# Kernel tuning notes

Hardware: AMD Instinct MI355X
Metric: run time of the kernel (lower is better)

Reference implementation:

```python
import jax, jax.numpy as jnp
import numpy as np
import math

EPS = 1e-12


def _cmul(ar, ai, br, bi):
    return ar * br - ai * bi, ar * bi + ai * br


def _wilson_seed(x):
    # x: (B, 4, L, L) -> conj of canonical Wilson-line path, (B, L, L) re/im
    ux_r, ux_i, uy_r, uy_i = x[:, 0], x[:, 1], x[:, 2], x[:, 3]
    B, L, _ = ux_r.shape
    dt = x.dtype

    def step(c, u):
        cr, ci = c
        ur, ui = u
        nr, ni = _cmul(cr, ci, ur, ui)
        return (nr, ni), (nr, ni)

    # cumulative complex product along x at y=0
    init_r = jnp.ones((B,), dt)
    init_i = jnp.zeros((B,), dt)
    xs = (ux_r[:, :-1, 0].T, ux_i[:, :-1, 0].T)  # (L-1, B)
    _, (axr, axi) = jax.lax.scan(step, (init_r, init_i), xs)
    x_axis_r = jnp.concatenate([init_r[None], axr], 0).T  # (B, L)
    x_axis_i = jnp.concatenate([init_i[None], axi], 0).T

    # cumulative complex product along y, vectorized over x
    ys = (jnp.moveaxis(uy_r[:, :, :-1], 2, 0), jnp.moveaxis(uy_i[:, :, :-1], 2, 0))  # (L-1, B, L)
    _, (pr, pi_) = jax.lax.scan(step, (x_axis_r, x_axis_i), ys)
    path_r = jnp.moveaxis(jnp.concatenate([x_axis_r[None], pr], 0), 0, 2)  # (B, L, L)
    path_i = jnp.moveaxis(jnp.concatenate([x_axis_i[None], pi_], 0), 0, 2)
    return path_r, -path_i  # conjugate


def _wrap(t):
    return (t + math.pi) % (2.0 * math.pi) - math.pi


def _initial_features(x):
    seed_r, seed_i = _wilson_seed(x)
    ax = jnp.arctan2(x[:, 1], x[:, 0])
    ay = jnp.arctan2(x[:, 3], x[:, 2])
    plaq = _wrap(ax + jnp.roll(ay, -1, axis=1) - jnp.roll(ax, -1, axis=2) - ay)
    pc = jnp.cos(plaq)
    pavg = (pc + jnp.roll(pc, 1, 1) + jnp.roll(pc, -1, 1)
            + jnp.roll(pc, 1, 2) + jnp.roll(pc, -1, 2)) / 5.0
    scalars = jnp.stack([jnp.ones_like(pc), pc, pavg], axis=1)  # (B, 3, L, L)
    return seed_r[:, None] * scalars, seed_i[:, None] * scalars


def _transport_fwd(fr, fi, x, mu):
    lr, li = (x[:, 0], x[:, 1]) if mu == 0 else (x[:, 2], x[:, 3])
    sr = jnp.roll(fr, -1, axis=mu + 2)
    si = jnp.roll(fi, -1, axis=mu + 2)
    return _cmul(lr[:, None], li[:, None], sr, si)


def _transport_bwd(fr, fi, x, mu):
    lr, li = (x[:, 0], x[:, 1]) if mu == 0 else (x[:, 2], x[:, 3])
    cr = jnp.roll(lr, 1, axis=mu + 1)
    ci = jnp.roll(-li, 1, axis=mu + 1)
    sr = jnp.roll(fr, 1, axis=mu + 2)
    si = jnp.roll(fi, 1, axis=mu + 2)
    return _cmul(cr[:, None], ci[:, None], sr, si)


def _lconv(fr, fi, x, center, fwd_w, bwd_w):
    out_r = jnp.einsum('oi,bixy->boxy', center, fr)
    out_i = jnp.einsum('oi,bixy->boxy', center, fi)
    for mu in range(2):
        fr2, fi2 = _transport_fwd(fr, fi, x, mu)
        br2, bi2 = _transport_bwd(fr, fi, x, mu)
        out_r = out_r + jnp.einsum('oi,bixy->boxy', fwd_w[mu], fr2) \
                      + jnp.einsum('oi,bixy->boxy', bwd_w[mu], br2)
        out_i = out_i + jnp.einsum('oi,bixy->boxy', fwd_w[mu], fi2) \
                      + jnp.einsum('oi,bixy->boxy', bwd_w[mu], bi2)
    return out_r, out_i


def _modrelu(fr, fi, bias):
    mag = jnp.sqrt(fr * fr + fi * fi + EPS)
    act = jax.nn.relu(mag + bias[None, :, None, None])
    scale = act / jnp.maximum(mag, EPS)
    return fr * scale, fi * scale


def setup_inputs() -> dict:
    key = jax.random.key(0)
    ks = jax.random.split(key, 11)
    B, L, H, O = 64, 128, 16, 8
    s = 0.1
    return {
        'x': jax.random.normal(ks[0], (B, 4, L, L), jnp.float32),
        'center1': s * jax.random.normal(ks[1], (H, 3), jnp.float32),
        'fwd_w1': s * jax.random.normal(ks[2], (2, H, 3), jnp.float32),
        'bwd_w1': s * jax.random.normal(ks[3], (2, H, 3), jnp.float32),
        'bias1': jnp.zeros((H,), jnp.float32),
        'center2': s * jax.random.normal(ks[4], (O, H), jnp.float32),
        'fwd_w2': s * jax.random.normal(ks[5], (2, O, H), jnp.float32),
        'bwd_w2': s * jax.random.normal(ks[6], (2, O, H), jnp.float32),
        'bias2': jnp.zeros((O,), jnp.float32),
        'ro_weight': s * jax.random.normal(ks[7], (O,), jnp.float32),
        'ro_bias': jnp.zeros((1,), jnp.float32),
    }


def reference(x, center1, fwd_w1, bwd_w1, bias1, center2, fwd_w2, bwd_w2, bias2, ro_weight, ro_bias):
    fr, fi = _initial_features(x)
    fr, fi = _lconv(fr, fi, x, center1, fwd_w1, bwd_w1)
    fr, fi = _modrelu(fr, fi, bias1)
    fr, fi = _lconv(fr, fi, x, center2, fwd_w2, bwd_w2)
    fr, fi = _modrelu(fr, fi, bias2)
    inv = fr * fr + fi * fi
    return jnp.einsum('c,bcxy->bxy', ro_weight, inv)[:, None] + ro_bias.reshape(1, 1, 1, 1)
```

## Files before the change

### kernel.cpp

```cpp
#include <hip/hip_runtime.h>
#include <math.h>

#define LQ   128
#define BQ   64
#define LL   (LQ*LQ)
#define H1   16
#define O2   8
#define TILE 16
#define REG  18
#define NPTS (REG*REG)
#define PCR  22
#define PCN  (PCR*PCR)
#define LKR  23
#define LKN  (LKR*LKR)

typedef float f2 __attribute__((ext_vector_type(2)));
using bf8 = __attribute__((ext_vector_type(8))) short;
using f4  = __attribute__((ext_vector_type(4))) float;

__device__ __forceinline__ int wrapi(int v) { return v & (LQ - 1); }

__device__ __forceinline__ unsigned pack_bf(float hi, float lo) {
    return __builtin_amdgcn_perm(__float_as_uint(hi), __float_as_uint(lo),
                                 0x07060302u);
}
__device__ __forceinline__ unsigned cvt_pk_bf16(float lo, float hi) {
    unsigned r;
    asm("v_cvt_pk_bf16_f32 %0, %1, %2" : "=v"(r) : "v"(lo), "v"(hi));
    return r;
}

#define WS_W1 ((size_t)BQ * LL)

__global__ __launch_bounds__(256)
void k_scan(const float* __restrict__ x,
            const float* __restrict__ c1, const float* __restrict__ fw1,
            const float* __restrict__ bw1, float* __restrict__ ws) {
    int blk = blockIdx.x;
    if (blk == BQ * 8) {
        int tid = threadIdx.x;
        if (tid < 120) {
            int t = tid / 24, r = tid - t * 24;
            int c = r >> 3, op = r & 7;
            const float* src = (t == 0) ? c1 : (t == 1) ? fw1 : (t == 2) ? bw1
                             : (t == 3) ? (fw1 + 48) : (bw1 + 48);
            float2 v = make_float2(src[(2 * op) * 3 + c], src[(2 * op + 1) * 3 + c]);
            ((float2*)ws)[WS_W1 + tid] = v;
        }
        return;
    }
    int b = blk >> 3, rq = blk & 7;
    int l = threadIdx.x & 63, w = threadIdx.x >> 6;
    const float* x0 = x + (size_t)b * 4 * LL;
    const float* x1 = x0 + LL;

    float ur0 = x0[(2 * l) * LQ],     ui0 = x1[(2 * l) * LQ];
    float ur1 = x0[(2 * l + 1) * LQ], ui1 = x1[(2 * l + 1) * LQ];
    float pr = ur0 * ur1 - ui0 * ui1;
    float pi = ur0 * ui1 + ui0 * ur1;
    for (int d = 1; d < 64; d <<= 1) {
        float qr = __shfl_up(pr, d, 64);
        float qi = __shfl_up(pi, d, 64);
        if (l >= d) {
            float nr = qr * pr - qi * pi;
            float ni = qr * pi + qi * pr;
            pr = nr; pi = ni;
        }
    }
    float er = __shfl_up(pr, 1, 64);
    float ei = __shfl_up(pi, 1, 64);
    if (l == 0) { er = 1.f; ei = 0.f; }
    float e1r = er * ur0 - ei * ui0;
    float e1i = er * ui0 + ei * ur0;

    const float* yrp = x + (size_t)(b * 4 + 2) * LL;
    const float* yip = yrp + LL;
    float4* seed4 = (float4*)ws;

    for (int k = 0; k < 4; ++k) {
        int i = rq * 16 + w * 4 + k;
        float cxr = __shfl((i & 1) ? e1r : er, i >> 1, 64);
        float cxi = __shfl((i & 1) ? e1i : ei, i >> 1, 64);
        const float* yr = yrp + (size_t)i * LQ;
        const float* yi = yip + (size_t)i * LQ;
        float vr0 = yr[2 * l],     vi0 = yi[2 * l];
        float vr1 = yr[2 * l + 1], vi1 = yi[2 * l + 1];
        float sr = vr0 * vr1 - vi0 * vi1;
        float si = vr0 * vi1 + vi0 * vr1;
        for (int d = 1; d < 64; d <<= 1) {
            float qr = __shfl_up(sr, d, 64);
            float qi = __shfl_up(si, d, 64);
            if (l >= d) {
                float nr = qr * sr - qi * si;
                float ni = qr * si + qi * sr;
                sr = nr; si = ni;
            }
        }
        float gr = __shfl_up(sr, 1, 64);
        float gi = __shfl_up(si, 1, 64);
        if (l == 0) { gr = 1.f; gi = 0.f; }
        float s0r = cxr * gr - cxi * gi;
        float s0i = cxr * gi + cxi * gr;
        float s1r = s0r * vr0 - s0i * vi0;
        float s1i = s0r * vi0 + s0i * vr0;
        seed4[((size_t)b * LL + (size_t)i * LQ) / 2 + l] =
            make_float4(s0r, -s0i, s1r, -s1i);
    }
}

__global__ __launch_bounds__(256, 5)
void k_main(const float* __restrict__ x,
            const float* __restrict__ c2, const float* __restrict__ fw2,
            const float* __restrict__ bw2, const float* __restrict__ b1,
            const float* __restrict__ b2,
            const float* __restrict__ ro, const float* __restrict__ rob,
            const float* __restrict__ ws, float* __restrict__ out) {
    __shared__ __align__(16) unsigned s_f1[NPTS * 16];
    __shared__ f2 s_ux[LKN];
    __shared__ f2 s_uy[LKN];
    __shared__ float s_pc[PCN];
    int tid = threadIdx.x;
    int b = blockIdx.z, i0 = blockIdx.y * TILE, j0 = blockIdx.x * TILE;
    const float* x0 = x + (size_t)b * 4 * LL;
    const float* x1 = x0 + LL;
    const float* x2 = x0 + 2 * LL;
    const float* x3 = x0 + 3 * LL;
    const float2* seed = (const float2*)ws + (size_t)b * LL;
    const float2* W1 = (const float2*)ws + WS_W1;

    int lane = tid & 63, w = tid >> 6;
    int kc = lane >> 4, h = lane & 15, half = kc >> 1;

    bool z1 = true;
#pragma unroll
    for (int hh = 0; hh < H1; ++hh) z1 = z1 && (b1[hh] == 0.f);
    bool z2 = true;
#pragma unroll
    for (int oo = 0; oo < O2; ++oo) z2 = z2 && (b2[oo] == 0.f);

    bf8 a1 = {0, 0, 0, 0, 0, 0, 0, 0};
    if (kc < 2) {
        float v[8];
#pragma unroll
        for (int j = 0; j < 8; ++j) {
            int k = kc * 8 + j;
            float val = 0.f;
            if (k < 15) {
                int q = k / 3, c = k - q * 3;
                val = ((const float*)(W1 + (q * 24 + c * 8 + (h >> 1))))[h & 1];
            }
            v[j] = val;
        }
        unsigned dw[4];
#pragma unroll
        for (int d = 0; d < 4; ++d) dw[d] = cvt_pk_bf16(v[2 * d], v[2 * d + 1]);
        __builtin_memcpy(&a1, dw, 16);
    }

    for (int p = tid; p < LKN; p += 256) {
        int ri = p / LKR, rj = p - ri * LKR;
        int gi = wrapi(i0 - 3 + ri), gj = wrapi(j0 - 3 + rj);
        int idx = gi * LQ + gj;
        s_ux[p] = (f2){x0[idx], x1[idx]};
        s_uy[p] = (f2){x2[idx], x3[idx]};
    }
    __syncthreads();

    for (int p = tid; p < PCN; p += 256) {
        int ri = p / PCR, rj = p - ri * PCR;
        int lb = ri * LKR + rj;
        f2 u1 = s_ux[lb];
        f2 u2 = s_uy[lb + LKR];
        f2 u3 = s_ux[lb + 1];
        f2 u4 = s_uy[lb];
        float ar = u1.x * u2.x - u1.y * u2.y, ai = u1.x * u2.y + u1.y * u2.x;
        float br = ar * u3.x + ai * u3.y,     bi = -ar * u3.y + ai * u3.x;
        float zr = br * u4.x + bi * u4.y,     zi = -br * u4.y + bi * u4.x;
        s_pc[p] = zr * __frsqrt_rn(fmaf(zr, zr, zi * zi) + 1e-30f);
    }
    __syncthreads();

    for (int wp = w * 64; wp < NPTS; wp += 256) {
        int p = wp + lane;
        int pp = (p < NPTS) ? p : (NPTS - 1);
        int ri = pp / REG, rj = pp - ri * REG;
        int lb = (ri + 2) * LKR + (rj + 2);
        int cb = (ri + 2) * PCR + (rj + 2);

        int gi0 = wrapi(i0 - 1 + ri), gim = wrapi(i0 - 2 + ri), gip = wrapi(i0 + ri);
        int gj0 = wrapi(j0 - 1 + rj), gjm = wrapi(j0 - 2 + rj), gjp = wrapi(j0 + rj);
        float2 SC  = seed[gi0 * LQ + gj0];
        float2 SXP = seed[gip * LQ + gj0];
        float2 SXM = seed[gim * LQ + gj0];
        float2 SYP = seed[gi0 * LQ + gjp];
        float2 SYM = seed[gi0 * LQ + gjm];

        f2 lx = s_ux[lb], ly = s_uy[lb];
        f2 mx = s_ux[lb - LKR], my = s_uy[lb - 1];
        float tr[5], ti[5], tc[5], tv[5];
        tr[0] = SC.x;                          ti[0] = SC.y;
        tr[1] = lx.x * SXP.x - lx.y * SXP.y;   ti[1] = lx.x * SXP.y + lx.y * SXP.x;
        tr[2] = mx.x * SXM.x + mx.y * SXM.y;   ti[2] = mx.x * SXM.y - mx.y * SXM.x;
        tr[3] = ly.x * SYP.x - ly.y * SYP.y;   ti[3] = ly.x * SYP.y + ly.y * SYP.x;
        tr[4] = my.x * SYM.x + my.y * SYM.y;   ti[4] = my.x * SYM.y - my.y * SYM.x;

        float p00 = s_pc[cb];
        float pP0 = s_pc[cb + PCR],     pM0 = s_pc[cb - PCR];
        float p0P = s_pc[cb + 1],       p0M = s_pc[cb - 1];
        float pP20 = s_pc[cb + 2*PCR],  pM20 = s_pc[cb - 2*PCR];
        float p0P2 = s_pc[cb + 2],      p0M2 = s_pc[cb - 2];
        float pPP = s_pc[cb + PCR + 1], pPM = s_pc[cb + PCR - 1];
        float pMP = s_pc[cb - PCR + 1], pMM = s_pc[cb - PCR - 1];
        tc[0] = p00; tc[1] = pP0; tc[2] = pM0; tc[3] = p0P; tc[4] = p0M;
        tv[0] = (p00 + pP0 + pM0 + p0P + p0M) * 0.2f;
        tv[1] = (pP0 + pP20 + p00 + pPP + pPM) * 0.2f;
        tv[2] = (pM0 + p00 + pM20 + pMP + pMM) * 0.2f;
        tv[3] = (p0P + pPP + pMP + p0P2 + p00) * 0.2f;
        tv[4] = (p0M + pPM + pMM + p00 + p0M2) * 0.2f;

        unsigned fr8[8], fi8[8];
        {
            float Fr[16], Fi[16];
#pragma unroll
            for (int q = 0; q < 5; ++q) {
                Fr[3*q]   = tr[q];         Fi[3*q]   = ti[q];
                Fr[3*q+1] = tc[q]*tr[q];   Fi[3*q+1] = tc[q]*ti[q];
                Fr[3*q+2] = tv[q]*tr[q];   Fi[3*q+2] = tv[q]*ti[q];
            }
            Fr[15] = 0.f; Fi[15] = 0.f;
#pragma unroll
            for (int d = 0; d < 8; ++d) {
                fr8[d] = cvt_pk_bf16(Fr[2*d], Fr[2*d+1]);
                fi8[d] = cvt_pk_bf16(Fi[2*d], Fi[2*d+1]);
            }
        }

        int ng = (NPTS - wp + 15) >> 4;
        if (ng > 4) ng = 4;
        for (int g = 0; g < ng; ++g) {
            int src = g * 16 + h;
            unsigned brw[4], biw[4];
#pragma unroll
            for (int d = 0; d < 4; ++d) {
                unsigned rlo = __shfl(fr8[d],     src, 64);
                unsigned rhi = __shfl(fr8[d + 4], src, 64);
                unsigned ilo = __shfl(fi8[d],     src, 64);
                unsigned ihi = __shfl(fi8[d + 4], src, 64);
                brw[d] = (kc == 0) ? rlo : ((kc == 1) ? rhi : 0u);
                biw[d] = (kc == 0) ? ilo : ((kc == 1) ? ihi : 0u);
            }
            bf8 br, bi;
            __builtin_memcpy(&br, brw, 16);
            __builtin_memcpy(&bi, biw, 16);
            f4 zc = {0.f, 0.f, 0.f, 0.f};
            f4 Dr = __builtin_amdgcn_mfma_f32_16x16x32_bf16(a1, br, zc, 0, 0, 0);
            f4 Di = __builtin_amdgcn_mfma_f32_16x16x32_bf16(a1, bi, zc, 0, 0, 0);
            int P = wp + g * 16 + h;
            if (P < NPTS) {
                if (!z1) {
#pragma unroll
                    for (int r = 0; r < 4; ++r) {
                        float q2 = Dr[r]*Dr[r] + Di[r]*Di[r] + 1e-12f;
                        float s = fmaxf(fmaf(b1[4*kc + r], __frsqrt_rn(q2), 1.f), 0.f);
                        Dr[r] *= s; Di[r] *= s;
                    }
                }
                unsigned pr0 = cvt_pk_bf16(Dr[0], Dr[1]);
                unsigned pr1 = cvt_pk_bf16(Dr[2], Dr[3]);
                unsigned pi0 = cvt_pk_bf16(Di[0], Di[1]);
                unsigned pi1 = cvt_pk_bf16(Di[2], Di[3]);
                int rot = (P >> 1) & 3;
                int base = P * 16 + ((kc & 1) << 1);
                int ar = base + ((((kc >> 1) + rot) & 3) << 2);
                int ai = base + ((((kc >> 1) + 2 + rot) & 3) << 2);
                *(uint2*)&s_f1[ar] = make_uint2(pr0, pr1);
                *(uint2*)&s_f1[ai] = make_uint2(pi0, pi1);
            }
        }
    }
    __syncthreads();

    const float* wLo[3] = {c2, bw2, bw2 + O2 * H1};
    const float* wHi[3] = {fw2, fw2 + O2 * H1, (const float*)0};
    bf8 afr[3];
#pragma unroll
    for (int pq = 0; pq < 3; ++pq) {
        bf8 z = {0, 0, 0, 0, 0, 0, 0, 0};
        const float* wsrc = half ? wHi[pq] : wLo[pq];
        int wrow = half ? (h - 8) : h;
        bool valid = half ? (h >= 8 && wsrc != 0) : (h < 8);
        if (valid) {
            const float* wp2 = wsrc + wrow * H1 + (kc & 1) * 8;
            float4 wa = *(const float4*)wp2;
            float4 wb = *(const float4*)(wp2 + 4);
            uint4 u;
            u.x = pack_bf(wa.y, wa.x);
            u.y = pack_bf(wa.w, wa.z);
            u.z = pack_bf(wb.y, wb.x);
            u.w = pack_bf(wb.w, wb.z);
            __builtin_memcpy(&z, &u, 16);
        }
        afr[pq] = z;
    }
    float4 ro_lo = *(const float4*)ro;
    float4 ro_hi = *(const float4*)(ro + 4);
    float4 b2_lo = *(const float4*)b2;
    float4 b2_hi = *(const float4*)(b2 + 4);
    float4 zf4 = make_float4(0.f, 0.f, 0.f, 0.f);
    float4 rv = (kc == 0) ? ro_lo : ((kc == 1) ? ro_hi : zf4);
    float4 bv = (kc == 0) ? b2_lo : ((kc == 1) ? b2_hi : zf4);
    float rob0 = rob[0];

    for (int g = 0; g < 4; ++g) {
        int row = w * 4 + g;
        int posc = (row + 1) * REG + (h + 1);
        int lb2 = (row + 3) * LKR + (h + 3);
        f2 lx = s_ux[lb2], ly = s_uy[lb2];
        f2 mx = s_ux[lb2 - LKR], my = s_uy[lb2 - 1];

        float Lr[3], Li[3];
        Lr[0] = half ? lx.x : 1.f;   Li[0] = half ? lx.y : 0.f;
        Lr[1] = half ? ly.x : mx.x;  Li[1] = half ? ly.y : -mx.y;
        Lr[2] = half ? 0.f : my.x;   Li[2] = half ? 0.f : -my.y;
        int dpl[3];
        dpl[0] = half ? REG : 0;
        dpl[1] = half ? 1 : -REG;
        dpl[2] = -1;

        f4 a2r = {0.f, 0.f, 0.f, 0.f}, a2i = {0.f, 0.f, 0.f, 0.f};
#pragma unroll
        for (int pq = 0; pq < 3; ++pq) {
            int posc2 = posc + dpl[pq];
            int rot2 = (posc2 >> 1) & 3;
            int bb = posc2 * 16;
            uint4 ur = *(const uint4*)&s_f1[bb + ((((kc & 1) + rot2) & 3) << 2)];
            uint4 ui = *(const uint4*)&s_f1[bb + ((((kc & 1) + 2 + rot2) & 3) << 2)];
            bf8 br, bi;
            __builtin_memcpy(&br, &ur, 16);
            __builtin_memcpy(&bi, &ui, 16);
            f4 zc = {0.f, 0.f, 0.f, 0.f};
            f4 sr = __builtin_amdgcn_mfma_f32_16x16x32_bf16(afr[pq], br, zc, 0, 0, 0);
            f4 si = __builtin_amdgcn_mfma_f32_16x16x32_bf16(afr[pq], bi, zc, 0, 0, 0);
            a2r += Lr[pq] * sr - Li[pq] * si;
            a2i += Lr[pq] * si + Li[pq] * sr;
        }

#pragma unroll
        for (int c = 0; c < 4; ++c) {
            a2r[c] += __shfl_xor(a2r[c], 32, 64);
            a2i[c] += __shfl_xor(a2i[c], 32, 64);
        }

        f4 q4 = a2r * a2r + a2i * a2i;
        float res;
        if (z2) {
            res = rv.x * q4.x + rv.y * q4.y + rv.z * q4.z + rv.w * q4.w;
        } else {
            float bvv[4] = {bv.x, bv.y, bv.z, bv.w};
            float rvv[4] = {rv.x, rv.y, rv.z, rv.w};
            res = 0.f;
#pragma unroll
            for (int r = 0; r < 4; ++r) {
                float qq = q4[r];
                float s = fmaxf(fmaf(bvv[r], __frsqrt_rn(qq + 1e-12f), 1.f), 0.f);
                res = fmaf(rvv[r], s * s * qq, res);
            }
        }
        res += __shfl_xor(res, 16, 64);
        if (kc == 0)
            out[(size_t)b * LL + (size_t)(i0 + row) * LQ + (j0 + h)] = res + rob0;
    }
}

extern "C" void kernel_launch(void* const* d_in, const int* in_sizes, int n_in,
                              void* d_out, int out_size, void* d_ws, size_t ws_size,
                              hipStream_t stream) {
    const float* x   = (const float*)d_in[0];
    const float* c1  = (const float*)d_in[1];
    const float* fw1 = (const float*)d_in[2];
    const float* bw1 = (const float*)d_in[3];
    const float* b1  = (const float*)d_in[4];
    const float* c2  = (const float*)d_in[5];
    const float* fw2 = (const float*)d_in[6];
    const float* bw2 = (const float*)d_in[7];
    const float* b2  = (const float*)d_in[8];
    const float* ro  = (const float*)d_in[9];
    const float* rob = (const float*)d_in[10];
    float* out = (float*)d_out;
    float* ws  = (float*)d_ws;

    k_scan<<<BQ * 8 + 1, 256, 0, stream>>>(x, c1, fw1, bw1, ws);
    dim3 grid(LQ / TILE, LQ / TILE, BQ);
    k_main<<<grid, 256, 0, stream>>>(x, c2, fw2, bw2, b1, b2,
                                     ro, rob, ws, out);
}
```

Baseline: 133.5 us.

## Widen main kernel to 512 threads, prepack bf16 weights, split feature build from MFMA

Both layers' weights are now converted to bf16 MFMA fragments once in the scan kernel's spare block and loaded directly by each lane. The main kernel moves to 512 threads, and the first-layer stage is split into two parts. A per-point feature build writes hi/lo bf16-split features to a wider, rotated shared buffer. A separate wave-distributed MFMA pass then reads them, replacing the earlier shuffle-based gather. The hi/lo split roughly doubles shared-memory traffic and storage for the features, and adds an extra barrier. In exchange it aims for higher parallelism and less per-block weight setup.

```diff
diff --git a/kernel.cpp b/kernel.cpp
--- a/kernel.cpp
+++ b/kernel.cpp
@@ -7,8 +7,13 @@
 #define H1   16
 #define O2   8
 #define TILE 16
+#define NTHR 512
+#define NWAVE 8
+#define RPW  2
 #define REG  18
 #define NPTS (REG*REG)
+#define NPTS_PAD 336
+#define NGRP 21
 #define PCR  22
 #define PCN  (PCR*PCR)
 #define LKR  23
@@ -20,32 +25,63 @@
 
 __device__ __forceinline__ int wrapi(int v) { return v & (LQ - 1); }
 
-__device__ __forceinline__ unsigned pack_bf(float hi, float lo) {
-    return __builtin_amdgcn_perm(__float_as_uint(hi), __float_as_uint(lo),
-                                 0x07060302u);
-}
 __device__ __forceinline__ unsigned cvt_pk_bf16(float lo, float hi) {
     unsigned r;
     asm("v_cvt_pk_bf16_f32 %0, %1, %2" : "=v"(r) : "v"(lo), "v"(hi));
     return r;
 }
 
-#define WS_W1 ((size_t)BQ * LL)
+#define WS_WF ((size_t)2 * BQ * LL)
 
 __global__ __launch_bounds__(256)
 void k_scan(const float* __restrict__ x,
             const float* __restrict__ c1, const float* __restrict__ fw1,
-            const float* __restrict__ bw1, float* __restrict__ ws) {
+            const float* __restrict__ bw1,
+            const float* __restrict__ c2, const float* __restrict__ fw2,
+            const float* __restrict__ bw2, float* __restrict__ ws) {
     int blk = blockIdx.x;
     if (blk == BQ * 8) {
         int tid = threadIdx.x;
-        if (tid < 120) {
-            int t = tid / 24, r = tid - t * 24;
-            int c = r >> 3, op = r & 7;
-            const float* src = (t == 0) ? c1 : (t == 1) ? fw1 : (t == 2) ? bw1
-                             : (t == 3) ? (fw1 + 48) : (bw1 + 48);
-            float2 v = make_float2(src[(2 * op) * 3 + c], src[(2 * op + 1) * 3 + c]);
-            ((float2*)ws)[WS_W1 + tid] = v;
+        uint4* wf = (uint4*)(ws + WS_WF);
+        if (tid < 64) {
+            int kc = tid >> 4, h = tid & 15;
+            unsigned dw[4];
+            float v[8];
+#pragma unroll
+            for (int j = 0; j < 8; ++j) {
+                int k = (kc & 1) * 8 + j;
+                float val = 0.f;
+                if (k < 15) {
+                    int q = k / 3, c = k - q * 3;
+                    const float* src = (q == 0) ? c1 : (q == 1) ? fw1
+                                     : (q == 2) ? bw1 : (q == 3) ? (fw1 + 48)
+                                     : (bw1 + 48);
+                    val = src[h * 3 + c];
+                }
+                v[j] = val;
+            }
+#pragma unroll
+            for (int d = 0; d < 4; ++d) dw[d] = cvt_pk_bf16(v[2*d], v[2*d+1]);
+            uint4 u = {dw[0], dw[1], dw[2], dw[3]};
+            wf[tid] = u;
+        } else {
+            int idx = tid - 64;
+            int pq = idx >> 6, lane = idx & 63;
+            int kc = lane >> 4, h = lane & 15, half = kc >> 1;
+            const float* wsrc = half
+                ? ((pq == 0) ? fw2 : (pq == 1) ? (fw2 + O2 * H1) : (const float*)0)
+                : ((pq == 0) ? c2  : (pq == 1) ? bw2 : (bw2 + O2 * H1));
+            unsigned dw[4] = {0u, 0u, 0u, 0u};
+            int wrow = half ? (h - 8) : h;
+            bool valid = half ? (h >= 8 && wsrc != 0) : (h < 8);
+            if (valid) {
+                const float* wp2 = wsrc + wrow * H1 + (kc & 1) * 8;
+#pragma unroll
+                for (int d = 0; d < 4; ++d)
+                    dw[d] = cvt_pk_bf16(wp2[2*d], wp2[2*d+1]);
+            }
+            uint4 u = {dw[0], dw[1], dw[2], dw[3]};
+            wf[64 + idx] = u;
         }
         return;
     }
@@ -108,14 +144,12 @@
     }
 }
 
-__global__ __launch_bounds__(256, 5)
+__global__ __launch_bounds__(NTHR, 6)
 void k_main(const float* __restrict__ x,
-            const float* __restrict__ c2, const float* __restrict__ fw2,
-            const float* __restrict__ bw2, const float* __restrict__ b1,
-            const float* __restrict__ b2,
+            const float* __restrict__ b1, const float* __restrict__ b2,
             const float* __restrict__ ro, const float* __restrict__ rob,
             const float* __restrict__ ws, float* __restrict__ out) {
-    __shared__ __align__(16) unsigned s_f1[NPTS * 16];
+    __shared__ __align__(16) unsigned s_f1[NPTS_PAD * 32];
     __shared__ f2 s_ux[LKN];
     __shared__ f2 s_uy[LKN];
     __shared__ float s_pc[PCN];
@@ -126,7 +160,7 @@
     const float* x2 = x0 + 2 * LL;
     const float* x3 = x0 + 3 * LL;
     const float2* seed = (const float2*)ws + (size_t)b * LL;
-    const float2* W1 = (const float2*)ws + WS_W1;
+    const uint4* wf = (const uint4*)(ws + WS_WF);
 
     int lane = tid & 63, w = tid >> 6;
     int kc = lane >> 4, h = lane & 15, half = kc >> 1;
@@ -138,26 +172,16 @@
 #pragma unroll
     for (int oo = 0; oo < O2; ++oo) z2 = z2 && (b2[oo] == 0.f);
 
-    bf8 a1 = {0, 0, 0, 0, 0, 0, 0, 0};
-    if (kc < 2) {
-        float v[8];
-#pragma unroll
-        for (int j = 0; j < 8; ++j) {
-            int k = kc * 8 + j;
-            float val = 0.f;
-            if (k < 15) {
-                int q = k / 3, c = k - q * 3;
-                val = ((const float*)(W1 + (q * 24 + c * 8 + (h >> 1))))[h & 1];
-            }
-            v[j] = val;
-        }
-        unsigned dw[4];
-#pragma unroll
-        for (int d = 0; d < 4; ++d) dw[d] = cvt_pk_bf16(v[2 * d], v[2 * d + 1]);
-        __builtin_memcpy(&a1, dw, 16);
-    }
-
-    for (int p = tid; p < LKN; p += 256) {
+    bf8 a1;
+    { uint4 u = wf[lane]; __builtin_memcpy(&a1, &u, 16); }
+    bf8 afr[3];
+#pragma unroll
+    for (int pq = 0; pq < 3; ++pq) {
+        uint4 u = wf[64 + pq * 64 + lane];
+        __builtin_memcpy(&afr[pq], &u, 16);
+    }
+
+    for (int p = tid; p < LKN; p += NTHR) {
         int ri = p / LKR, rj = p - ri * LKR;
         int gi = wrapi(i0 - 3 + ri), gj = wrapi(j0 - 3 + rj);
         int idx = gi * LQ + gj;
@@ -166,7 +190,7 @@
     }
     __syncthreads();
 
-    for (int p = tid; p < PCN; p += 256) {
+    for (int p = tid; p < PCN; p += NTHR) {
         int ri = p / PCR, rj = p - ri * PCR;
         int lb = ri * LKR + rj;
         f2 u1 = s_ux[lb];
@@ -180,46 +204,45 @@
     }
     __syncthreads();
 
-    for (int wp = w * 64; wp < NPTS; wp += 256) {
-        int p = wp + lane;
-        int pp = (p < NPTS) ? p : (NPTS - 1);
-        int ri = pp / REG, rj = pp - ri * REG;
-        int lb = (ri + 2) * LKR + (rj + 2);
-        int cb = (ri + 2) * PCR + (rj + 2);
-
-        int gi0 = wrapi(i0 - 1 + ri), gim = wrapi(i0 - 2 + ri), gip = wrapi(i0 + ri);
-        int gj0 = wrapi(j0 - 1 + rj), gjm = wrapi(j0 - 2 + rj), gjp = wrapi(j0 + rj);
-        float2 SC  = seed[gi0 * LQ + gj0];
-        float2 SXP = seed[gip * LQ + gj0];
-        float2 SXM = seed[gim * LQ + gj0];
-        float2 SYP = seed[gi0 * LQ + gjp];
-        float2 SYM = seed[gi0 * LQ + gjm];
-
-        f2 lx = s_ux[lb], ly = s_uy[lb];
-        f2 mx = s_ux[lb - LKR], my = s_uy[lb - 1];
-        float tr[5], ti[5], tc[5], tv[5];
-        tr[0] = SC.x;                          ti[0] = SC.y;
-        tr[1] = lx.x * SXP.x - lx.y * SXP.y;   ti[1] = lx.x * SXP.y + lx.y * SXP.x;
-        tr[2] = mx.x * SXM.x + mx.y * SXM.y;   ti[2] = mx.x * SXM.y - mx.y * SXM.x;
-        tr[3] = ly.x * SYP.x - ly.y * SYP.y;   ti[3] = ly.x * SYP.y + ly.y * SYP.x;
-        tr[4] = my.x * SYM.x + my.y * SYM.y;   ti[4] = my.x * SYM.y - my.y * SYM.x;
-
-        float p00 = s_pc[cb];
-        float pP0 = s_pc[cb + PCR],     pM0 = s_pc[cb - PCR];
-        float p0P = s_pc[cb + 1],       p0M = s_pc[cb - 1];
-        float pP20 = s_pc[cb + 2*PCR],  pM20 = s_pc[cb - 2*PCR];
-        float p0P2 = s_pc[cb + 2],      p0M2 = s_pc[cb - 2];
-        float pPP = s_pc[cb + PCR + 1], pPM = s_pc[cb + PCR - 1];
-        float pMP = s_pc[cb - PCR + 1], pMM = s_pc[cb - PCR - 1];
-        tc[0] = p00; tc[1] = pP0; tc[2] = pM0; tc[3] = p0P; tc[4] = p0M;
-        tv[0] = (p00 + pP0 + pM0 + p0P + p0M) * 0.2f;
-        tv[1] = (pP0 + pP20 + p00 + pPP + pPM) * 0.2f;
-        tv[2] = (pM0 + p00 + pM20 + pMP + pMM) * 0.2f;
-        tv[3] = (p0P + pPP + pMP + p0P2 + p00) * 0.2f;
-        tv[4] = (p0M + pPM + pMM + p00 + p0M2) * 0.2f;
-
-        unsigned fr8[8], fi8[8];
-        {
+    for (int p = tid; p < NPTS_PAD; p += NTHR) {
+        int rot = p & 7;
+        unsigned* dst = &s_f1[p * 32];
+        if (p < NPTS) {
+            int ri = p / REG, rj = p - ri * REG;
+            int lb = (ri + 2) * LKR + (rj + 2);
+            int cb = (ri + 2) * PCR + (rj + 2);
+
+            int gi0 = wrapi(i0 - 1 + ri), gim = wrapi(i0 - 2 + ri), gip = wrapi(i0 + ri);
+            int gj0 = wrapi(j0 - 1 + rj), gjm = wrapi(j0 - 2 + rj), gjp = wrapi(j0 + rj);
+            float2 SC  = seed[gi0 * LQ + gj0];
+            float2 SXP = seed[gip * LQ + gj0];
+            float2 SXM = seed[gim * LQ + gj0];
+            float2 SYP = seed[gi0 * LQ + gjp];
+            float2 SYM = seed[gi0 * LQ + gjm];
+
+            f2 lx = s_ux[lb], ly = s_uy[lb];
+            f2 mx = s_ux[lb - LKR], my = s_uy[lb - 1];
+            float tr[5], ti[5], tc[5], tv[5];
+            tr[0] = SC.x;                          ti[0] = SC.y;
+            tr[1] = lx.x * SXP.x - lx.y * SXP.y;   ti[1] = lx.x * SXP.y + lx.y * SXP.x;
+            tr[2] = mx.x * SXM.x + mx.y * SXM.y;   ti[2] = mx.x * SXM.y - mx.y * SXM.x;
+            tr[3] = ly.x * SYP.x - ly.y * SYP.y;   ti[3] = ly.x * SYP.y + ly.y * SYP.x;
+            tr[4] = my.x * SYM.x + my.y * SYM.y;   ti[4] = my.x * SYM.y - my.y * SYM.x;
+
+            float p00 = s_pc[cb];
+            float pP0 = s_pc[cb + PCR],     pM0 = s_pc[cb - PCR];
+            float p0P = s_pc[cb + 1],       p0M = s_pc[cb - 1];
+            float pP20 = s_pc[cb + 2*PCR],  pM20 = s_pc[cb - 2*PCR];
+            float p0P2 = s_pc[cb + 2],      p0M2 = s_pc[cb - 2];
+            float pPP = s_pc[cb + PCR + 1], pPM = s_pc[cb + PCR - 1];
+            float pMP = s_pc[cb - PCR + 1], pMM = s_pc[cb - PCR - 1];
+            tc[0] = p00; tc[1] = pP0; tc[2] = pM0; tc[3] = p0P; tc[4] = p0M;
+            tv[0] = (p00 + pP0 + pM0 + p0P + p0M) * 0.2f;
+            tv[1] = (pP0 + pP20 + p00 + pPP + pPM) * 0.2f;
+            tv[2] = (pM0 + p00 + pM20 + pMP + pMM) * 0.2f;
+            tv[3] = (p0P + pPP + pMP + p0P2 + p00) * 0.2f;
+            tv[4] = (p0M + pPM + pMM + p00 + p0M2) * 0.2f;
+
             float Fr[16], Fi[16];
 #pragma unroll
             for (int q = 0; q < 5; ++q) {
@@ -228,80 +251,77 @@
                 Fr[3*q+2] = tv[q]*tr[q];   Fi[3*q+2] = tv[q]*ti[q];
             }
             Fr[15] = 0.f; Fi[15] = 0.f;
+            unsigned hr[8], hi_[8], lr[8], li_[8];
 #pragma unroll
             for (int d = 0; d < 8; ++d) {
-                fr8[d] = cvt_pk_bf16(Fr[2*d], Fr[2*d+1]);
-                fi8[d] = cvt_pk_bf16(Fi[2*d], Fi[2*d+1]);
-            }
-        }
-
-        int ng = (NPTS - wp + 15) >> 4;
-        if (ng > 4) ng = 4;
-        for (int g = 0; g < ng; ++g) {
-            int src = g * 16 + h;
-            unsigned brw[4], biw[4];
-#pragma unroll
-            for (int d = 0; d < 4; ++d) {
-                unsigned rlo = __shfl(fr8[d],     src, 64);
-                unsigned rhi = __shfl(fr8[d + 4], src, 64);
-                unsigned ilo = __shfl(fi8[d],     src, 64);
-                unsigned ihi = __shfl(fi8[d + 4], src, 64);
-                brw[d] = (kc == 0) ? rlo : ((kc == 1) ? rhi : 0u);
-                biw[d] = (kc == 0) ? ilo : ((kc == 1) ? ihi : 0u);
-            }
-            bf8 br, bi;
-            __builtin_memcpy(&br, brw, 16);
-            __builtin_memcpy(&bi, biw, 16);
-            f4 zc = {0.f, 0.f, 0.f, 0.f};
-            f4 Dr = __builtin_amdgcn_mfma_f32_16x16x32_bf16(a1, br, zc, 0, 0, 0);
-            f4 Di = __builtin_amdgcn_mfma_f32_16x16x32_bf16(a1, bi, zc, 0, 0, 0);
-            int P = wp + g * 16 + h;
-            if (P < NPTS) {
-                if (!z1) {
-#pragma unroll
-                    for (int r = 0; r < 4; ++r) {
-                        float q2 = Dr[r]*Dr[r] + Di[r]*Di[r] + 1e-12f;
-                        float s = fmaxf(fmaf(b1[4*kc + r], __frsqrt_rn(q2), 1.f), 0.f);
-                        Dr[r] *= s; Di[r] *= s;
-                    }
+                hr[d]  = cvt_pk_bf16(Fr[2*d], Fr[2*d+1]);
+                hi_[d] = cvt_pk_bf16(Fi[2*d], Fi[2*d+1]);
+                float r0 = Fr[2*d]   - __uint_as_float(hr[d] << 16);
+                float r1 = Fr[2*d+1] - __uint_as_float(hr[d] & 0xFFFF0000u);
+                float q0 = Fi[2*d]   - __uint_as_float(hi_[d] << 16);
+                float q1 = Fi[2*d+1] - __uint_as_float(hi_[d] & 0xFFFF0000u);
+                lr[d]  = cvt_pk_bf16(r0, r1);
+                li_[d] = cvt_pk_bf16(q0, q1);
+            }
+            uint4 vs0 = {hr[0], hr[1], hr[2], hr[3]};
+            uint4 vs1 = {hr[4], hr[5], hr[6], hr[7]};
+            uint4 vs2 = {hi_[0], hi_[1], hi_[2], hi_[3]};
+            uint4 vs3 = {hi_[4], hi_[5], hi_[6], hi_[7]};
+            uint4 vs4 = {lr[0], lr[1], lr[2], lr[3]};
+            uint4 vs5 = {lr[4], lr[5], lr[6], lr[7]};
+            uint4 vs6 = {li_[0], li_[1], li_[2], li_[3]};
+            uint4 vs7 = {li_[4], li_[5], li_[6], li_[7]};
+            *(uint4*)&dst[((0 + rot) & 7) * 4] = vs0;
+            *(uint4*)&dst[((1 + rot) & 7) * 4] = vs1;
+            *(uint4*)&dst[((2 + rot) & 7) * 4] = vs2;
+            *(uint4*)&dst[((3 + rot) & 7) * 4] = vs3;
+            *(uint4*)&dst[((4 + rot) & 7) * 4] = vs4;
+            *(uint4*)&dst[((5 + rot) & 7) * 4] = vs5;
+            *(uint4*)&dst[((6 + rot) & 7) * 4] = vs6;
+            *(uint4*)&dst[((7 + rot) & 7) * 4] = vs7;
+        } else {
+            uint4 z = {0u, 0u, 0u, 0u};
+#pragma unroll
+            for (int s = 0; s < 8; ++s) *(uint4*)&dst[s * 4] = z;
+        }
+    }
+    __syncthreads();
+
+    for (int g = w; g < NGRP; g += NWAVE) {
+        int P = g * 16 + h;
+        int rot = P & 7;
+        unsigned* bb = &s_f1[P * 32];
+        int sr = (kc < 2) ? kc : (kc + 2);
+        uint4 ur = *(const uint4*)&bb[((sr + rot) & 7) * 4];
+        uint4 ui = *(const uint4*)&bb[((sr + 2 + rot) & 7) * 4];
+        bf8 br, bi;
+        __builtin_memcpy(&br, &ur, 16);
+        __builtin_memcpy(&bi, &ui, 16);
+        f4 zc = {0.f, 0.f, 0.f, 0.f};
+        f4 Dr = __builtin_amdgcn_mfma_f32_16x16x32_bf16(a1, br, zc, 0, 0, 0);
+        f4 Di = __builtin_amdgcn_mfma_f32_16x16x32_bf16(a1, bi, zc, 0, 0, 0);
+        if (P < NPTS) {
+            if (!z1) {
+#pragma unroll
+                for (int r = 0; r < 4; ++r) {
+                    float q2 = Dr[r]*Dr[r] + Di[r]*Di[r] + 1e-12f;
+                    float s = fmaxf(fmaf(b1[4*kc + r], __frsqrt_rn(q2), 1.f), 0.f);
+                    Dr[r] *= s; Di[r] *= s;
                 }
-                unsigned pr0 = cvt_pk_bf16(Dr[0], Dr[1]);
-                unsigned pr1 = cvt_pk_bf16(Dr[2], Dr[3]);
-                unsigned pi0 = cvt_pk_bf16(Di[0], Di[1]);
-                unsigned pi1 = cvt_pk_bf16(Di[2], Di[3]);
-                int rot = (P >> 1) & 3;
-                int base = P * 16 + ((kc & 1) << 1);
-                int ar = base + ((((kc >> 1) + rot) & 3) << 2);
-                int ai = base + ((((kc >> 1) + 2 + rot) & 3) << 2);
-                *(uint2*)&s_f1[ar] = make_uint2(pr0, pr1);
-                *(uint2*)&s_f1[ai] = make_uint2(pi0, pi1);
-            }
+            }
+            unsigned pr0 = cvt_pk_bf16(Dr[0], Dr[1]);
+            unsigned pr1 = cvt_pk_bf16(Dr[2], Dr[3]);
+            unsigned pi0 = cvt_pk_bf16(Di[0], Di[1]);
+            unsigned pi1 = cvt_pk_bf16(Di[2], Di[3]);
+            int base = P * 32 + ((kc & 1) << 1);
+            int ar = base + ((((kc >> 1) + rot) & 7) << 2);
+            int ai = base + ((((kc >> 1) + 2 + rot) & 7) << 2);
+            *(uint2*)&s_f1[ar] = make_uint2(pr0, pr1);
+            *(uint2*)&s_f1[ai] = make_uint2(pi0, pi1);
         }
     }
     __syncthreads();
 
-    const float* wLo[3] = {c2, bw2, bw2 + O2 * H1};
-    const float* wHi[3] = {fw2, fw2 + O2 * H1, (const float*)0};
-    bf8 afr[3];
-#pragma unroll
-    for (int pq = 0; pq < 3; ++pq) {
-        bf8 z = {0, 0, 0, 0, 0, 0, 0, 0};
-        const float* wsrc = half ? wHi[pq] : wLo[pq];
-        int wrow = half ? (h - 8) : h;
-        bool valid = half ? (h >= 8 && wsrc != 0) : (h < 8);
-        if (valid) {
-            const float* wp2 = wsrc + wrow * H1 + (kc & 1) * 8;
-            float4 wa = *(const float4*)wp2;
-            float4 wb = *(const float4*)(wp2 + 4);
-            uint4 u;
-            u.x = pack_bf(wa.y, wa.x);
-            u.y = pack_bf(wa.w, wa.z);
-            u.z = pack_bf(wb.y, wb.x);
-            u.w = pack_bf(wb.w, wb.z);
-            __builtin_memcpy(&z, &u, 16);
-        }
-        afr[pq] = z;
-    }
     float4 ro_lo = *(const float4*)ro;
     float4 ro_hi = *(const float4*)(ro + 4);
     float4 b2_lo = *(const float4*)b2;
@@ -311,8 +331,8 @@
     float4 bv = (kc == 0) ? b2_lo : ((kc == 1) ? b2_hi : zf4);
     float rob0 = rob[0];
 
-    for (int g = 0; g < 4; ++g) {
-        int row = w * 4 + g;
+    for (int g = 0; g < RPW; ++g) {
+        int row = w * RPW + g;
         int posc = (row + 1) * REG + (h + 1);
         int lb2 = (row + 3) * LKR + (h + 3);
         f2 lx = s_ux[lb2], ly = s_uy[lb2];
@@ -331,10 +351,10 @@
 #pragma unroll
         for (int pq = 0; pq < 3; ++pq) {
             int posc2 = posc + dpl[pq];
-            int rot2 = (posc2 >> 1) & 3;
-            int bb = posc2 * 16;
-            uint4 ur = *(const uint4*)&s_f1[bb + ((((kc & 1) + rot2) & 3) << 2)];
-            uint4 ui = *(const uint4*)&s_f1[bb + ((((kc & 1) + 2 + rot2) & 3) << 2)];
+            int rot2 = posc2 & 7;
+            int bb = posc2 * 32;
+            uint4 ur = *(const uint4*)&s_f1[bb + ((((kc & 1) + rot2) & 7) << 2)];
+            uint4 ui = *(const uint4*)&s_f1[bb + ((((kc & 1) + 2 + rot2) & 7) << 2)];
             bf8 br, bi;
             __builtin_memcpy(&br, &ur, 16);
             __builtin_memcpy(&bi, &ui, 16);
@@ -389,8 +409,7 @@
     float* out = (float*)d_out;
     float* ws  = (float*)d_ws;
 
-    k_scan<<<BQ * 8 + 1, 256, 0, stream>>>(x, c1, fw1, bw1, ws);
+    k_scan<<<BQ * 8 + 1, 256, 0, stream>>>(x, c1, fw1, bw1, c2, fw2, bw2, ws);
     dim3 grid(LQ / TILE, LQ / TILE, BQ);
-    k_main<<<grid, 256, 0, stream>>>(x, c2, fw2, bw2, b1, b2,
-                                     ro, rob, ws, out);
+    k_main<<<grid, NTHR, 0, stream>>>(x, b1, b2, ro, rob, ws, out);
 }
```

Measured after the change: 127.7 us. 4.3% less time.
